# Kernel optimization log

Hardware: AMD Instinct MI355X
Metric: run time of the kernel (lower is better)

## Reference

```python
import jax, jax.numpy as jnp
import numpy as np

BH, S, D = 32, 2048, 128

def setup_inputs() -> dict:
    key = jax.random.key(0)
    k1, k2, k3 = jax.random.split(key, 3)
    return {
        "key": jax.random.normal(k1, (BH, S, D), dtype=jnp.float32),
        "query": jax.random.normal(k2, (BH, S, D), dtype=jnp.float32),
        "value": jax.random.normal(k3, (BH, S, D), dtype=jnp.float32),
    }

def reference(key, query, value):
    # scores = Q K^T / sqrt(d)  -> softmax over keys -> @ V
    scale = 1.0 / np.sqrt(key.shape[-1]).astype(np.float32)
    scores = jnp.einsum('bqd,bkd->bqk', query, key) * scale  # [BH, S, S]
    probs = jax.nn.softmax(scores, axis=-1)
    return jnp.einsum('bqk,bkd->bqd', probs, value)  # [BH, S, D]
```

## Files before the change

### kernel.cpp

```cpp
#include <hip/hip_runtime.h>
#include <hip/hip_bf16.h>
#include <cmath>

#define BH_N 32
#define SEQ  2048
#define DH   128
#define BM   256
#define KT   64
#define NTILES (SEQ / KT)

typedef __attribute__((ext_vector_type(4)))  float f32x4;
typedef __attribute__((ext_vector_type(16))) float f32x16;
typedef __attribute__((ext_vector_type(8)))  short bf16x8;
typedef __attribute__((ext_vector_type(4)))  unsigned int u32x4;

__device__ __forceinline__ unsigned cvtpk(float lo, float hi) {
  unsigned r;
  asm("v_cvt_pk_bf16_f32 %0, %1, %2" : "=v"(r) : "v"(lo), "v"(hi));
  return r;
}


__global__ __launch_bounds__(512, 2) void attn_fwd(
    const float* __restrict__ Kg, const float* __restrict__ Qg,
    const float* __restrict__ Vg, float* __restrict__ Og)
{
  __shared__ __align__(16) char lds[65536];
  constexpr float QSC = 0.08838834764831845f * 1.4426950408889634f;

  const int t    = threadIdx.x;
  const int lane = t & 63;
  const int w    = t >> 6;
  const int hi   = lane >> 5;
  const int q31  = lane & 31;

  const int bid = blockIdx.x;
  const int lb  = (bid & 7) * 32 + (bid >> 3);
  const int bh  = lb >> 3;
  const int qb  = lb & 7;
  const int blkq = qb * BM;
  const size_t base = (size_t)bh * SEQ * DH;

  bf16x8 qf[8];
  {
    const float* qp = Qg + base + (size_t)(blkq + w * 32 + q31) * DH + hi * 8;
    #pragma unroll
    for (int s = 0; s < 8; ++s) {
      const float4 a = *(const float4*)(qp + s * 16);
      const float4 b = *(const float4*)(qp + s * 16 + 4);
      u32x4 u = { cvtpk(a.x * QSC, a.y * QSC), cvtpk(a.z * QSC, a.w * QSC),
                  cvtpk(b.x * QSC, b.y * QSC), cvtpk(b.z * QSC, b.w * QSC) };
      qf[s] = __builtin_bit_cast(bf16x8, u);
    }
  }

  const int kq = t >> 4;
  const int kd = (t & 15) * 8;
  const int vd = t & 127;
  const int vk = (t >> 7) * 16;
  const float* kp0 = Kg + base + (size_t)kq * DH + kd;
  const float* vp0 = Vg + base + (size_t)vk * DH + vd;

  auto kv_load = [&](int tile2, float4* kf4, float* vv) {
    const float* kp = kp0 + (size_t)tile2 * (KT * DH);
    kf4[0] = *(const float4*)kp;
    kf4[1] = *(const float4*)(kp + 4);
    kf4[2] = *(const float4*)(kp + 32 * DH);
    kf4[3] = *(const float4*)(kp + 32 * DH + 4);
    const float* vp = vp0 + (size_t)tile2 * (KT * DH);
    #pragma unroll
    for (int j = 0; j < 16; ++j) vv[j] = vp[j * DH];
  };
  auto k_write = [&](char* bb, const float4* kf4) {
    #pragma unroll
    for (int i = 0; i < 2; ++i) {
      const int key = kq + i * 32;
      u32x4 u = { cvtpk(kf4[2*i].x, kf4[2*i].y), cvtpk(kf4[2*i].z, kf4[2*i].w),
                  cvtpk(kf4[2*i+1].x, kf4[2*i+1].y), cvtpk(kf4[2*i+1].z, kf4[2*i+1].w) };
      *(u32x4*)(bb + key * 256 + ((kd * 2) ^ ((key & 15) << 4))) = u;
    }
  };
  auto v_write = [&](char* bb, const float* vv) {
    const int rr = vd & 63;
    const int hb = (vd >> 6) << 7;
    const int sw = (vd & 15) << 4;
    u32x4 u0 = { cvtpk(vv[0], vv[1]),  cvtpk(vv[2], vv[3]),
                 cvtpk(vv[4], vv[5]),  cvtpk(vv[6], vv[7]) };
    u32x4 u1 = { cvtpk(vv[8], vv[9]),  cvtpk(vv[10], vv[11]),
                 cvtpk(vv[12], vv[13]), cvtpk(vv[14], vv[15]) };
    char* rowp = bb + 16384 + rr * 256;
    *(u32x4*)(rowp + ((hb + vk * 2) ^ sw))      = u0;
    *(u32x4*)(rowp + ((hb + vk * 2 + 16) ^ sw)) = u1;
  };

  f32x16 ot[4];
  #pragma unroll
  for (int dt = 0; dt < 4; ++dt)
    #pragma unroll
    for (int r = 0; r < 16; ++r) ot[dt][r] = 0.f;

  float l_run = 0.f;

  {
    float4 kf4[4]; float vv[16];
    kv_load(0, kf4, vv);
    k_write(lds, kf4); v_write(lds, vv);
  }
  __syncthreads();

  for (int tile = 0; tile < NTILES; ++tile) {
    char* cbp = lds + (tile & 1) * 32768;
    char* nbp = lds + ((tile + 1) & 1) * 32768;
    float4 kf4[4]; float vv[16];
    const bool pre = (tile + 1 < NTILES);
    if (pre) kv_load(tile + 1, kf4, vv);

    f32x16 st[2];
    #pragma unroll
    for (int kt = 0; kt < 2; ++kt)
      #pragma unroll
      for (int r = 0; r < 16; ++r) st[kt][r] = 0.f;
    __builtin_amdgcn_s_setprio(1);
    #pragma unroll
    for (int kt = 0; kt < 2; ++kt) {
      const int row = kt * 32 + q31;
      const int ksw = (row & 15) << 4;
      char* rb = cbp + row * 256;
      #pragma unroll
      for (int ks = 0; ks < 8; ++ks) {
        const bf16x8 kf = *(const bf16x8*)(rb + ((ks * 32 + hi * 16) ^ ksw));
        st[kt] = __builtin_amdgcn_mfma_f32_32x32x16_bf16(kf, qf[ks], st[kt], 0, 0, 0);
      }
    }
    __builtin_amdgcn_s_setprio(0);

    float psum = 0.f;
    #pragma unroll
    for (int kt = 0; kt < 2; ++kt)
      #pragma unroll
      for (int r = 0; r < 16; ++r) {
        const float p = exp2f(st[kt][r]);
        st[kt][r] = p;
        psum += p;
      }
    psum += __shfl_xor(psum, 32);
    l_run += psum;

    bf16x8 pf[4];
    #pragma unroll
    for (int kt = 0; kt < 2; ++kt) {
      unsigned a0 = cvtpk(st[kt][0], st[kt][1]);
      unsigned b0 = cvtpk(st[kt][4], st[kt][5]);
      asm volatile("v_permlane32_swap_b32 %0, %1" : "+v"(a0), "+v"(b0));
      unsigned c0 = cvtpk(st[kt][2], st[kt][3]);
      unsigned d0 = cvtpk(st[kt][6], st[kt][7]);
      asm volatile("v_permlane32_swap_b32 %0, %1" : "+v"(c0), "+v"(d0));
      u32x4 ue = { a0, c0, b0, d0 };
      pf[2 * kt] = __builtin_bit_cast(bf16x8, ue);
      unsigned a1 = cvtpk(st[kt][8],  st[kt][9]);
      unsigned b1 = cvtpk(st[kt][12], st[kt][13]);
      asm volatile("v_permlane32_swap_b32 %0, %1" : "+v"(a1), "+v"(b1));
      unsigned c1 = cvtpk(st[kt][10], st[kt][11]);
      unsigned d1 = cvtpk(st[kt][14], st[kt][15]);
      asm volatile("v_permlane32_swap_b32 %0, %1" : "+v"(c1), "+v"(d1));
      u32x4 uo = { a1, c1, b1, d1 };
      pf[2 * kt + 1] = __builtin_bit_cast(bf16x8, uo);
    }

    if (pre) k_write(nbp, kf4);

    __builtin_amdgcn_s_setprio(1);
    #pragma unroll
    for (int ks = 0; ks < 4; ++ks)
      #pragma unroll
      for (int dt = 0; dt < 4; ++dt) {
        const int d  = dt * 32 + q31;
        const int rr = d & 63;
        const int off = 16384 + rr * 256 +
                        ((((d >> 6) << 7) + ks * 32 + hi * 16) ^ ((d & 15) << 4));
        const bf16x8 vf = *(const bf16x8*)(cbp + off);
        ot[dt] = __builtin_amdgcn_mfma_f32_32x32x16_bf16(vf, pf[ks], ot[dt], 0, 0, 0);
      }
    __builtin_amdgcn_s_setprio(0);

    if (pre) v_write(nbp, vv);
    __syncthreads();
  }

  const float rcp = 1.0f / l_run;
  char* ep = lds + (w << 12);
  const int qsw = (q31 & 7) << 4;
  const int qr  = lane >> 1;
  const int hf  = lane & 1;
  const int rsw = (qr & 7) << 4;
  float* orow = Og + base + (size_t)(blkq + w * 32) * DH;
  #pragma unroll
  for (int dt = 0; dt < 4; ++dt) {
    #pragma unroll
    for (int a = 0; a < 4; ++a) {
      f32x4 v = { ot[dt][4*a+0] * rcp, ot[dt][4*a+1] * rcp,
                  ot[dt][4*a+2] * rcp, ot[dt][4*a+3] * rcp };
      const int dl = 8 * a + 4 * hi;
      *(f32x4*)(ep + q31 * 128 + ((dl * 4) ^ qsw)) = v;
    }
    float* op = orow + (size_t)qr * DH + dt * 32 + hf * 16;
    #pragma unroll
    for (int u = 0; u < 4; ++u) {
      const f32x4 v = *(const f32x4*)(ep + qr * 128 + ((hf * 64 + u * 16) ^ rsw));
      *(f32x4*)(op + u * 4) = v;
    }
    __syncthreads();
  }
}

extern "C" void kernel_launch(void* const* d_in, const int* in_sizes, int n_in,
                              void* d_out, int out_size, void* d_ws, size_t ws_size,
                              hipStream_t stream) {
  const float* Kg = (const float*)d_in[0];
  const float* Qg = (const float*)d_in[1];
  const float* Vg = (const float*)d_in[2];
  float* Og = (float*)d_out;
  attn_fwd<<<dim3(BH_N * (SEQ / BM)), dim3(512), 0, stream>>>(Kg, Qg, Vg, Og);
}
```

Measured before the change: 102.1 us.

## Prepack K/V to swizzled bf16 in workspace and stream via direct global-to-LDS loads

Adds a prepack kernel that converts K and V once per call into bf16 chunks with the swizzled LDS layout and stores them in the workspace. The main kernel then stages each tile with global_load_lds, so no register round-trip or per-block fp32 conversion is needed. It also splits keys across two wave groups per 128-query block, with a cross-wave reduction of outputs and row sums at the end, and doubles the grid. The cost is an extra kernel launch plus a workspace write and read, and the result depends on the workspace size check; a fallback keeps the old kernel.

```diff
diff --git a/kernel.cpp b/kernel.cpp
--- a/kernel.cpp
+++ b/kernel.cpp
@@ -5,9 +5,10 @@
 #define BH_N 32
 #define SEQ  2048
 #define DH   128
-#define BM   256
 #define KT   64
 #define NTILES (SEQ / KT)
+#define CHUNK 32768
+#define WS_NEED ((size_t)BH_N * NTILES * CHUNK)
 
 typedef __attribute__((ext_vector_type(4)))  float f32x4;
 typedef __attribute__((ext_vector_type(16))) float f32x16;
@@ -20,10 +21,47 @@
   return r;
 }
 
-
-__global__ __launch_bounds__(512, 2) void attn_fwd(
-    const float* __restrict__ Kg, const float* __restrict__ Qg,
-    const float* __restrict__ Vg, float* __restrict__ Og)
+typedef const __attribute__((address_space(1))) unsigned int* gas_u32;
+typedef __attribute__((address_space(3))) unsigned int* las_u32;
+__device__ __forceinline__ void gload_lds16(const void* g, void* l) {
+  __builtin_amdgcn_global_load_lds((gas_u32)g, (las_u32)l, 16, 0, 0);
+}
+
+__global__ __launch_bounds__(256) void prepack(
+    const float* __restrict__ Kg, const float* __restrict__ Vg, char* __restrict__ ws)
+{
+  const int cid = blockIdx.x;
+  const int bh = cid >> 5, tl = cid & 31;
+  const int kb = tl * KT;
+  const size_t base = (size_t)bh * SEQ * DH;
+  char* out = ws + (size_t)cid * CHUNK;
+  const int t = threadIdx.x;
+
+  #pragma unroll
+  for (int i = 0; i < 4; ++i) {
+    const int s = t + 256 * i;
+    const int key = s >> 4, j = s & 15;
+    const float* p = Kg + base + (size_t)(kb + key) * DH + j * 8;
+    const float4 a = *(const float4*)p;
+    const float4 b = *(const float4*)(p + 4);
+    u32x4 u = { cvtpk(a.x, a.y), cvtpk(a.z, a.w), cvtpk(b.x, b.y), cvtpk(b.z, b.w) };
+    *(u32x4*)(out + key * 256 + ((j * 16) ^ ((key & 15) << 4))) = u;
+  }
+  #pragma unroll
+  for (int i = 0; i < 4; ++i) {
+    const int s = t + 256 * i;
+    const int rr = s & 63, h = (s >> 6) & 1, k0 = (s >> 7) * 8;
+    const int d = rr + 64 * h;
+    const float* p = Vg + base + (size_t)(kb + k0) * DH + d;
+    const float v0 = p[0*DH], v1 = p[1*DH], v2 = p[2*DH], v3 = p[3*DH];
+    const float v4 = p[4*DH], v5 = p[5*DH], v6 = p[6*DH], v7 = p[7*DH];
+    u32x4 u = { cvtpk(v0, v1), cvtpk(v2, v3), cvtpk(v4, v5), cvtpk(v6, v7) };
+    *(u32x4*)(out + 16384 + rr * 256 + ((h * 128 + k0 * 2) ^ ((rr & 15) << 4))) = u;
+  }
+}
+
+__global__ __launch_bounds__(512, 4) void attn_main(
+    const float* __restrict__ Qg, const char* __restrict__ ws, float* __restrict__ Og)
 {
   __shared__ __align__(16) char lds[65536];
   constexpr float QSC = 0.08838834764831845f * 1.4426950408889634f;
@@ -31,19 +69,22 @@
   const int t    = threadIdx.x;
   const int lane = t & 63;
   const int w    = t >> 6;
+  const int qs   = w & 3;
+  const int kh   = w >> 2;
   const int hi   = lane >> 5;
   const int q31  = lane & 31;
 
   const int bid = blockIdx.x;
-  const int lb  = (bid & 7) * 32 + (bid >> 3);
-  const int bh  = lb >> 3;
-  const int qb  = lb & 7;
-  const int blkq = qb * BM;
+  const int lb  = (bid & 7) * 64 + (bid >> 3);
+  const int bh  = lb >> 4;
+  const int qb  = lb & 15;
+  const int blkq = qb * 128;
   const size_t base = (size_t)bh * SEQ * DH;
+  const char* wsb = ws + (size_t)(bh * NTILES) * CHUNK;
 
   bf16x8 qf[8];
   {
-    const float* qp = Qg + base + (size_t)(blkq + w * 32 + q31) * DH + hi * 8;
+    const float* qp = Qg + base + (size_t)(blkq + qs * 32 + q31) * DH + hi * 8;
     #pragma unroll
     for (int s = 0; s < 8; ++s) {
       const float4 a = *(const float4*)(qp + s * 16);
@@ -54,19 +95,175 @@
     }
   }
 
-  const int kq = t >> 4;
-  const int kd = (t & 15) * 8;
-  const int vd = t & 127;
-  const int vk = (t >> 7) * 16;
+  auto stage = [&](int tile, int buf) {
+    const char* src = wsb + (size_t)tile * CHUNK + (w * 4096) + lane * 16;
+    char* dst = lds + buf + w * 4096;
+    #pragma unroll
+    for (int r = 0; r < 4; ++r)
+      gload_lds16(src + r * 1024, dst + r * 1024);
+  };
+
+  f32x16 ot[4];
+  #pragma unroll
+  for (int dt = 0; dt < 4; ++dt)
+    #pragma unroll
+    for (int r = 0; r < 16; ++r) ot[dt][r] = 0.f;
+  float l_run = 0.f;
+
+  stage(0, 0);
+  __syncthreads();
+
+  const int krow = kh * 32 + q31;
+  const int ksw  = (krow & 15) << 4;
+
+  for (int tile = 0; tile < NTILES; ++tile) {
+    const int cb = (tile & 1) << 15;
+    if (tile + 1 < NTILES) stage(tile + 1, cb ^ 32768);
+
+    f32x16 st;
+    #pragma unroll
+    for (int r = 0; r < 16; ++r) st[r] = 0.f;
+    const char* rb = lds + cb + krow * 256;
+    __builtin_amdgcn_s_setprio(1);
+    #pragma unroll
+    for (int ks = 0; ks < 8; ++ks) {
+      const bf16x8 kf = *(const bf16x8*)(rb + ((ks * 32 + hi * 16) ^ ksw));
+      st = __builtin_amdgcn_mfma_f32_32x32x16_bf16(kf, qf[ks], st, 0, 0, 0);
+    }
+    __builtin_amdgcn_s_setprio(0);
+
+    float psum = 0.f;
+    #pragma unroll
+    for (int r = 0; r < 16; ++r) {
+      const float p = exp2f(st[r]);
+      st[r] = p;
+      psum += p;
+    }
+    psum += __shfl_xor(psum, 32);
+    l_run += psum;
+
+    bf16x8 pf[2];
+    {
+      unsigned a0 = cvtpk(st[0], st[1]);
+      unsigned b0 = cvtpk(st[4], st[5]);
+      asm volatile("v_permlane32_swap_b32 %0, %1" : "+v"(a0), "+v"(b0));
+      unsigned c0 = cvtpk(st[2], st[3]);
+      unsigned d0 = cvtpk(st[6], st[7]);
+      asm volatile("v_permlane32_swap_b32 %0, %1" : "+v"(c0), "+v"(d0));
+      u32x4 ue = { a0, c0, b0, d0 };
+      pf[0] = __builtin_bit_cast(bf16x8, ue);
+      unsigned a1 = cvtpk(st[8],  st[9]);
+      unsigned b1 = cvtpk(st[12], st[13]);
+      asm volatile("v_permlane32_swap_b32 %0, %1" : "+v"(a1), "+v"(b1));
+      unsigned c1 = cvtpk(st[10], st[11]);
+      unsigned d1 = cvtpk(st[14], st[15]);
+      asm volatile("v_permlane32_swap_b32 %0, %1" : "+v"(c1), "+v"(d1));
+      u32x4 uo = { a1, c1, b1, d1 };
+      pf[1] = __builtin_bit_cast(bf16x8, uo);
+    }
+
+    __builtin_amdgcn_s_setprio(1);
+    #pragma unroll
+    for (int ks2 = 0; ks2 < 2; ++ks2)
+      #pragma unroll
+      for (int dt = 0; dt < 4; ++dt) {
+        const int d  = dt * 32 + q31;
+        const int rr = d & 63;
+        const int off = 16384 + rr * 256 +
+            ((((d >> 6) << 7) + kh * 64 + ks2 * 32 + hi * 16) ^ ((d & 15) << 4));
+        const bf16x8 vf = *(const bf16x8*)(lds + cb + off);
+        ot[dt] = __builtin_amdgcn_mfma_f32_32x32x16_bf16(vf, pf[ks2], ot[dt], 0, 0, 0);
+      }
+    __builtin_amdgcn_s_setprio(0);
+
+    __syncthreads();
+  }
+
+  float* lfs = (float*)lds;
+  if (kh) lfs[qs * 64 + lane] = l_run;
+  __syncthreads();
+  float rcp = 0.f;
+  if (!kh) rcp = 1.0f / (l_run + lfs[qs * 64 + lane]);
+  __syncthreads();
+  const int dsw = (lane & 15) << 4;
+  if (kh) {
+    char* dp = lds + qs * 16384 + lane * 256;
+    #pragma unroll
+    for (int dt = 0; dt < 4; ++dt)
+      #pragma unroll
+      for (int a = 0; a < 4; ++a) {
+        f32x4 v = { ot[dt][4*a+0], ot[dt][4*a+1], ot[dt][4*a+2], ot[dt][4*a+3] };
+        *(f32x4*)(dp + ((dt * 64 + a * 16) ^ dsw)) = v;
+      }
+  }
+  __syncthreads();
+  if (!kh) {
+    char* dp = lds + qs * 16384 + lane * 256;
+    #pragma unroll
+    for (int dt = 0; dt < 4; ++dt)
+      #pragma unroll
+      for (int a = 0; a < 4; ++a) {
+        const f32x4 v = *(const f32x4*)(dp + ((dt * 64 + a * 16) ^ dsw));
+        ot[dt][4*a+0] = (ot[dt][4*a+0] + v[0]) * rcp;
+        ot[dt][4*a+1] = (ot[dt][4*a+1] + v[1]) * rcp;
+        ot[dt][4*a+2] = (ot[dt][4*a+2] + v[2]) * rcp;
+        ot[dt][4*a+3] = (ot[dt][4*a+3] + v[3]) * rcp;
+      }
+    char* ep = lds + qs * 16384;
+    const int qsw = (q31 & 7) << 4;
+    const int qr  = lane >> 1;
+    const int hf  = lane & 1;
+    const int rsw = (qr & 7) << 4;
+    float* orow = Og + base + (size_t)(blkq + qs * 32) * DH;
+    #pragma unroll
+    for (int dt = 0; dt < 4; ++dt) {
+      #pragma unroll
+      for (int a = 0; a < 4; ++a) {
+        f32x4 v = { ot[dt][4*a+0], ot[dt][4*a+1], ot[dt][4*a+2], ot[dt][4*a+3] };
+        const int dl = 8 * a + 4 * hi;
+        *(f32x4*)(ep + q31 * 128 + ((dl * 4) ^ qsw)) = v;
+      }
+      float* op = orow + (size_t)qr * DH + dt * 32 + hf * 16;
+      #pragma unroll
+      for (int u = 0; u < 4; ++u) {
+        const f32x4 v = *(const f32x4*)(ep + qr * 128 + ((hf * 64 + u * 16) ^ rsw));
+        *(f32x4*)(op + u * 4) = v;
+      }
+    }
+  }
+}
+
+__global__ __launch_bounds__(512, 2) void attn_fb(
+    const float* __restrict__ Kg, const float* __restrict__ Qg,
+    const float* __restrict__ Vg, float* __restrict__ Og)
+{
+  __shared__ __align__(16) char lds[65536];
+  constexpr float QSC = 0.08838834764831845f * 1.4426950408889634f;
+  const int t = threadIdx.x, lane = t & 63, w = t >> 6, hi = lane >> 5, q31 = lane & 31;
+  const int bid = blockIdx.x;
+  const int lb = (bid & 7) * 32 + (bid >> 3);
+  const int bh = lb >> 3, qb = lb & 7;
+  const int blkq = qb * 256;
+  const size_t base = (size_t)bh * SEQ * DH;
+  bf16x8 qf[8];
+  {
+    const float* qp = Qg + base + (size_t)(blkq + w * 32 + q31) * DH + hi * 8;
+    #pragma unroll
+    for (int s = 0; s < 8; ++s) {
+      const float4 a = *(const float4*)(qp + s * 16);
+      const float4 b = *(const float4*)(qp + s * 16 + 4);
+      u32x4 u = { cvtpk(a.x * QSC, a.y * QSC), cvtpk(a.z * QSC, a.w * QSC),
+                  cvtpk(b.x * QSC, b.y * QSC), cvtpk(b.z * QSC, b.w * QSC) };
+      qf[s] = __builtin_bit_cast(bf16x8, u);
+    }
+  }
+  const int kq = t >> 4, kd = (t & 15) * 8, vd = t & 127, vk = (t >> 7) * 16;
   const float* kp0 = Kg + base + (size_t)kq * DH + kd;
   const float* vp0 = Vg + base + (size_t)vk * DH + vd;
-
   auto kv_load = [&](int tile2, float4* kf4, float* vv) {
     const float* kp = kp0 + (size_t)tile2 * (KT * DH);
-    kf4[0] = *(const float4*)kp;
-    kf4[1] = *(const float4*)(kp + 4);
-    kf4[2] = *(const float4*)(kp + 32 * DH);
-    kf4[3] = *(const float4*)(kp + 32 * DH + 4);
+    kf4[0] = *(const float4*)kp; kf4[1] = *(const float4*)(kp + 4);
+    kf4[2] = *(const float4*)(kp + 32 * DH); kf4[3] = *(const float4*)(kp + 32 * DH + 4);
     const float* vp = vp0 + (size_t)tile2 * (KT * DH);
     #pragma unroll
     for (int j = 0; j < 16; ++j) vv[j] = vp[j * DH];
@@ -81,40 +278,27 @@
     }
   };
   auto v_write = [&](char* bb, const float* vv) {
-    const int rr = vd & 63;
-    const int hb = (vd >> 6) << 7;
-    const int sw = (vd & 15) << 4;
-    u32x4 u0 = { cvtpk(vv[0], vv[1]),  cvtpk(vv[2], vv[3]),
-                 cvtpk(vv[4], vv[5]),  cvtpk(vv[6], vv[7]) };
-    u32x4 u1 = { cvtpk(vv[8], vv[9]),  cvtpk(vv[10], vv[11]),
-                 cvtpk(vv[12], vv[13]), cvtpk(vv[14], vv[15]) };
+    const int rr = vd & 63, hb = (vd >> 6) << 7, sw = (vd & 15) << 4;
+    u32x4 u0 = { cvtpk(vv[0], vv[1]), cvtpk(vv[2], vv[3]), cvtpk(vv[4], vv[5]), cvtpk(vv[6], vv[7]) };
+    u32x4 u1 = { cvtpk(vv[8], vv[9]), cvtpk(vv[10], vv[11]), cvtpk(vv[12], vv[13]), cvtpk(vv[14], vv[15]) };
     char* rowp = bb + 16384 + rr * 256;
-    *(u32x4*)(rowp + ((hb + vk * 2) ^ sw))      = u0;
+    *(u32x4*)(rowp + ((hb + vk * 2) ^ sw)) = u0;
     *(u32x4*)(rowp + ((hb + vk * 2 + 16) ^ sw)) = u1;
   };
-
   f32x16 ot[4];
   #pragma unroll
   for (int dt = 0; dt < 4; ++dt)
     #pragma unroll
     for (int r = 0; r < 16; ++r) ot[dt][r] = 0.f;
-
   float l_run = 0.f;
-
-  {
-    float4 kf4[4]; float vv[16];
-    kv_load(0, kf4, vv);
-    k_write(lds, kf4); v_write(lds, vv);
-  }
+  { float4 kf4[4]; float vv[16]; kv_load(0, kf4, vv); k_write(lds, kf4); v_write(lds, vv); }
   __syncthreads();
-
   for (int tile = 0; tile < NTILES; ++tile) {
     char* cbp = lds + (tile & 1) * 32768;
     char* nbp = lds + ((tile + 1) & 1) * 32768;
     float4 kf4[4]; float vv[16];
     const bool pre = (tile + 1 < NTILES);
     if (pre) kv_load(tile + 1, kf4, vv);
-
     f32x16 st[2];
     #pragma unroll
     for (int kt = 0; kt < 2; ++kt)
@@ -133,19 +317,13 @@
       }
     }
     __builtin_amdgcn_s_setprio(0);
-
     float psum = 0.f;
     #pragma unroll
     for (int kt = 0; kt < 2; ++kt)
       #pragma unroll
-      for (int r = 0; r < 16; ++r) {
-        const float p = exp2f(st[kt][r]);
-        st[kt][r] = p;
-        psum += p;
-      }
+      for (int r = 0; r < 16; ++r) { const float p = exp2f(st[kt][r]); st[kt][r] = p; psum += p; }
     psum += __shfl_xor(psum, 32);
     l_run += psum;
-
     bf16x8 pf[4];
     #pragma unroll
     for (int kt = 0; kt < 2; ++kt) {
@@ -157,7 +335,7 @@
       asm volatile("v_permlane32_swap_b32 %0, %1" : "+v"(c0), "+v"(d0));
       u32x4 ue = { a0, c0, b0, d0 };
       pf[2 * kt] = __builtin_bit_cast(bf16x8, ue);
-      unsigned a1 = cvtpk(st[kt][8],  st[kt][9]);
+      unsigned a1 = cvtpk(st[kt][8], st[kt][9]);
       unsigned b1 = cvtpk(st[kt][12], st[kt][13]);
       asm volatile("v_permlane32_swap_b32 %0, %1" : "+v"(a1), "+v"(b1));
       unsigned c1 = cvtpk(st[kt][10], st[kt][11]);
@@ -166,15 +344,13 @@
       u32x4 uo = { a1, c1, b1, d1 };
       pf[2 * kt + 1] = __builtin_bit_cast(bf16x8, uo);
     }
-
     if (pre) k_write(nbp, kf4);
-
     __builtin_amdgcn_s_setprio(1);
     #pragma unroll
     for (int ks = 0; ks < 4; ++ks)
       #pragma unroll
       for (int dt = 0; dt < 4; ++dt) {
-        const int d  = dt * 32 + q31;
+        const int d = dt * 32 + q31;
         const int rr = d & 63;
         const int off = 16384 + rr * 256 +
                         ((((d >> 6) << 7) + ks * 32 + hi * 16) ^ ((d & 15) << 4));
@@ -182,16 +358,13 @@
         ot[dt] = __builtin_amdgcn_mfma_f32_32x32x16_bf16(vf, pf[ks], ot[dt], 0, 0, 0);
       }
     __builtin_amdgcn_s_setprio(0);
-
     if (pre) v_write(nbp, vv);
     __syncthreads();
   }
-
   const float rcp = 1.0f / l_run;
   char* ep = lds + (w << 12);
   const int qsw = (q31 & 7) << 4;
-  const int qr  = lane >> 1;
-  const int hf  = lane & 1;
+  const int qr = lane >> 1, hf = lane & 1;
   const int rsw = (qr & 7) << 4;
   float* orow = Og + base + (size_t)(blkq + w * 32) * DH;
   #pragma unroll
@@ -220,5 +393,11 @@
   const float* Qg = (const float*)d_in[1];
   const float* Vg = (const float*)d_in[2];
   float* Og = (float*)d_out;
-  attn_fwd<<<dim3(BH_N * (SEQ / BM)), dim3(512), 0, stream>>>(Kg, Qg, Vg, Og);
-}
+  if (ws_size >= WS_NEED) {
+    char* ws = (char*)d_ws;
+    prepack<<<dim3(BH_N * NTILES), dim3(256), 0, stream>>>(Kg, Vg, ws);
+    attn_main<<<dim3(BH_N * (SEQ / 128)), dim3(512), 0, stream>>>(Qg, ws, Og);
+  } else {
+    attn_fb<<<dim3(BH_N * (SEQ / 256)), dim3(512), 0, stream>>>(Kg, Qg, Vg, Og);
+  }
+}
```

Measured after the change: 133.2 us. 30.5% more time.

## Halve query block to 128 rows with 256 threads and vectorized K/V loads

Applied to the files above, without the earlier changes.

Cuts each block to 128 query rows and 4 waves, doubling the grid to 512 blocks and remapping the block index swizzle to match. Because half as many threads now stage each 64-key K/V tile, each thread loads twice as much. K is fetched as eight contiguous float4s and V as eight float4 rows, replacing sixteen scalar strided V loads, then transposed in registers before the bf16 LDS write. This aims to improve load efficiency and block scheduling across CUs, at the cost of reading each K/V tile twice as often per query row and using more registers per thread.

```diff
diff --git a/kernel.cpp b/kernel.cpp
--- a/kernel.cpp
+++ b/kernel.cpp
@@ -5,7 +5,7 @@
 #define BH_N 32
 #define SEQ  2048
 #define DH   128
-#define BM   256
+#define BM   128
 #define KT   64
 #define NTILES (SEQ / KT)
 
@@ -21,7 +21,7 @@
 }
 
 
-__global__ __launch_bounds__(512, 2) void attn_fwd(
+__global__ __launch_bounds__(256, 2) void attn_fwd(
     const float* __restrict__ Kg, const float* __restrict__ Qg,
     const float* __restrict__ Vg, float* __restrict__ Og)
 {
@@ -35,9 +35,9 @@
   const int q31  = lane & 31;
 
   const int bid = blockIdx.x;
-  const int lb  = (bid & 7) * 32 + (bid >> 3);
-  const int bh  = lb >> 3;
-  const int qb  = lb & 7;
+  const int lb  = (bid & 7) * 64 + (bid >> 3);
+  const int bh  = lb >> 4;
+  const int qb  = lb & 15;
   const int blkq = qb * BM;
   const size_t base = (size_t)bh * SEQ * DH;
 
@@ -54,43 +54,40 @@
     }
   }
 
-  const int kq = t >> 4;
-  const int kd = (t & 15) * 8;
-  const int vd = t & 127;
-  const int vk = (t >> 7) * 16;
-  const float* kp0 = Kg + base + (size_t)kq * DH + kd;
-  const float* vp0 = Vg + base + (size_t)vk * DH + vd;
-
-  auto kv_load = [&](int tile2, float4* kf4, float* vv) {
+  const int kq  = t >> 2;
+  const int kd0 = (t & 3) * 32;
+  const int vd4 = (t & 31) * 4;
+  const int vk8 = (t >> 5) * 8;
+  const float* kp0 = Kg + base + (size_t)kq * DH + kd0;
+  const float* vp0 = Vg + base + (size_t)vk8 * DH + vd4;
+
+  auto kv_load = [&](int tile2, float4* kf4, float4* vv4) {
     const float* kp = kp0 + (size_t)tile2 * (KT * DH);
-    kf4[0] = *(const float4*)kp;
-    kf4[1] = *(const float4*)(kp + 4);
-    kf4[2] = *(const float4*)(kp + 32 * DH);
-    kf4[3] = *(const float4*)(kp + 32 * DH + 4);
+    #pragma unroll
+    for (int j = 0; j < 8; ++j) kf4[j] = *(const float4*)(kp + j * 4);
     const float* vp = vp0 + (size_t)tile2 * (KT * DH);
     #pragma unroll
-    for (int j = 0; j < 16; ++j) vv[j] = vp[j * DH];
+    for (int j = 0; j < 8; ++j) vv4[j] = *(const float4*)(vp + (size_t)j * DH);
   };
   auto k_write = [&](char* bb, const float4* kf4) {
-    #pragma unroll
-    for (int i = 0; i < 2; ++i) {
-      const int key = kq + i * 32;
-      u32x4 u = { cvtpk(kf4[2*i].x, kf4[2*i].y), cvtpk(kf4[2*i].z, kf4[2*i].w),
-                  cvtpk(kf4[2*i+1].x, kf4[2*i+1].y), cvtpk(kf4[2*i+1].z, kf4[2*i+1].w) };
-      *(u32x4*)(bb + key * 256 + ((kd * 2) ^ ((key & 15) << 4))) = u;
+    const int sw = (kq & 15) << 4;
+    #pragma unroll
+    for (int m = 0; m < 4; ++m) {
+      u32x4 u = { cvtpk(kf4[2*m].x,   kf4[2*m].y),   cvtpk(kf4[2*m].z,   kf4[2*m].w),
+                  cvtpk(kf4[2*m+1].x, kf4[2*m+1].y), cvtpk(kf4[2*m+1].z, kf4[2*m+1].w) };
+      *(u32x4*)(bb + kq * 256 + ((kd0 * 2 + 16 * m) ^ sw)) = u;
     }
   };
-  auto v_write = [&](char* bb, const float* vv) {
-    const int rr = vd & 63;
-    const int hb = (vd >> 6) << 7;
-    const int sw = (vd & 15) << 4;
-    u32x4 u0 = { cvtpk(vv[0], vv[1]),  cvtpk(vv[2], vv[3]),
-                 cvtpk(vv[4], vv[5]),  cvtpk(vv[6], vv[7]) };
-    u32x4 u1 = { cvtpk(vv[8], vv[9]),  cvtpk(vv[10], vv[11]),
-                 cvtpk(vv[12], vv[13]), cvtpk(vv[14], vv[15]) };
-    char* rowp = bb + 16384 + rr * 256;
-    *(u32x4*)(rowp + ((hb + vk * 2) ^ sw))      = u0;
-    *(u32x4*)(rowp + ((hb + vk * 2 + 16) ^ sw)) = u1;
+  auto v_write = [&](char* bb, const float4* vv4) {
+    #pragma unroll
+    for (int r = 0; r < 4; ++r) {
+      const int d  = vd4 + r;
+      const int rr = d & 63;
+      const int hb = (d >> 6) << 7;
+      u32x4 u = { cvtpk(vv4[0][r], vv4[1][r]), cvtpk(vv4[2][r], vv4[3][r]),
+                  cvtpk(vv4[4][r], vv4[5][r]), cvtpk(vv4[6][r], vv4[7][r]) };
+      *(u32x4*)(bb + 16384 + rr * 256 + ((hb + vk8 * 2) ^ ((rr & 15) << 4))) = u;
+    }
   };
 
   f32x16 ot[4];
@@ -102,18 +99,18 @@
   float l_run = 0.f;
 
   {
-    float4 kf4[4]; float vv[16];
-    kv_load(0, kf4, vv);
-    k_write(lds, kf4); v_write(lds, vv);
+    float4 kf4[8], vv4[8];
+    kv_load(0, kf4, vv4);
+    k_write(lds, kf4); v_write(lds, vv4);
   }
   __syncthreads();
 
   for (int tile = 0; tile < NTILES; ++tile) {
     char* cbp = lds + (tile & 1) * 32768;
     char* nbp = lds + ((tile + 1) & 1) * 32768;
-    float4 kf4[4]; float vv[16];
+    float4 kf4[8], vv4[8];
     const bool pre = (tile + 1 < NTILES);
-    if (pre) kv_load(tile + 1, kf4, vv);
+    if (pre) kv_load(tile + 1, kf4, vv4);
 
     f32x16 st[2];
     #pragma unroll
@@ -183,7 +180,7 @@
       }
     __builtin_amdgcn_s_setprio(0);
 
-    if (pre) v_write(nbp, vv);
+    if (pre) v_write(nbp, vv4);
     __syncthreads();
   }
 
@@ -220,5 +217,5 @@
   const float* Qg = (const float*)d_in[1];
   const float* Vg = (const float*)d_in[2];
   float* Og = (float*)d_out;
-  attn_fwd<<<dim3(BH_N * (SEQ / BM)), dim3(512), 0, stream>>>(Kg, Qg, Vg, Og);
+  attn_fwd<<<dim3(BH_N * (SEQ / BM)), dim3(256), 0, stream>>>(Kg, Qg, Vg, Og);
 }
```

New measurement: 129.7 us. +27.1%, slower.
